# Optimization experiments

Hardware: AMD Instinct MI355X
Metric: run time of the kernel (lower is better)

Reference implementation:

```python
import jax, jax.numpy as jnp
import numpy as np

H, C, R, L = 4, 32, 4, 2   # heads, per-head dim, num_relations, num_layers
D = H * C                  # hidden_channels = in_channels = 128
EPS_BN = 1e-5
NEG_SLOPE = 0.2


def _forward(x0, src0, dst0, ea0, src1, dst1, ea1,
             Wl, Wr, bl, br, att, conv_b,
             bn_g, bn_b, bn_m, bn_v,
             skip_W, skip_b,
             proj_W, proj_b, pbn_g, pbn_b, pbn_m, pbn_v, prelu_a,
             n_t0, n_t1):
    x = x0
    layers = [(src0, dst0, ea0, n_t0), (src1, dst1, ea1, n_t1)]
    for i, (src, dst, ea, nt) in enumerate(layers):
        xt = x[:nt]                               # [nt, D] target nodes
        out = xt @ skip_W[i] + skip_b[i]          # skip connection
        for j in range(R):                        # per-relation GATv2 + BN (eval)
            mask = (ea == j)
            xl = (x @ Wl[i, j] + bl[i, j]).reshape(-1, H, C)   # [N, H, C]
            xr = (xt @ Wr[i, j] + br[i, j]).reshape(-1, H, C)  # [nt, H, C]
            msg = xl[src] + xr[dst]                            # [E, H, C]
            logit = jnp.sum(jax.nn.leaky_relu(msg, NEG_SLOPE) * att[i, j], axis=-1)  # [E, H]
            logit = jnp.where(mask[:, None], logit, -1e9)      # mask other relations
            amax = jax.ops.segment_max(logit, dst, num_segments=nt)                  # [nt, H]
            p = jnp.exp(logit - amax[dst]) * mask[:, None]
            denom = jax.ops.segment_sum(p, dst, num_segments=nt)
            alpha = p / jnp.maximum(denom, 1e-16)[dst]                               # [E, H]
            agg = jax.ops.segment_sum(alpha[..., None] * xl[src], dst, num_segments=nt)
            agg = agg.reshape(nt, D) + conv_b[i, j]
            out = out + (agg - bn_m[i, j]) * jax.lax.rsqrt(bn_v[i, j] + EPS_BN) * bn_g[i, j] + bn_b[i, j]
        x = jax.nn.elu(out)   # dropout is identity in eval mode
    # projection head: Linear -> BN(eval) -> PReLU -> Dropout(identity)
    h = x @ proj_W + proj_b
    h = (h - pbn_m) * jax.lax.rsqrt(pbn_v + EPS_BN) * pbn_g + pbn_b
    proj = jnp.where(h > 0, h, prelu_a * h)
    return x, proj


def setup_inputs() -> dict:
    key = jax.random.key(0)
    ks = jax.random.split(key, 32)
    N0, E0, N1, E1, N2 = 100000, 400000, 30000, 150000, 8000

    def w(k, shape, s=0.1):
        return jax.random.normal(k, shape, dtype=jnp.float32) * s

    return {
        'x0': jax.random.normal(ks[0], (N0, D), dtype=jnp.float32),
        'src0': jax.random.randint(ks[1], (E0,), 0, N0),
        'dst0': jax.random.randint(ks[2], (E0,), 0, N1),
        'ea0': jax.random.randint(ks[3], (E0,), 0, R),
        'src1': jax.random.randint(ks[4], (E1,), 0, N1),
        'dst1': jax.random.randint(ks[5], (E1,), 0, N2),
        'ea1': jax.random.randint(ks[6], (E1,), 0, R),
        'Wl': w(ks[7], (L, R, D, D)), 'Wr': w(ks[8], (L, R, D, D)),
        'bl': w(ks[9], (L, R, D)), 'br': w(ks[10], (L, R, D)),
        'att': w(ks[11], (L, R, H, C)), 'conv_b': w(ks[12], (L, R, D)),
        'bn_g': 1.0 + w(ks[13], (L, R, D)), 'bn_b': w(ks[14], (L, R, D)),
        'bn_m': w(ks[15], (L, R, D)),
        'bn_v': 0.5 + jax.random.uniform(ks[16], (L, R, D), dtype=jnp.float32),
        'skip_W': w(ks[17], (L, D, D)), 'skip_b': w(ks[18], (L, D)),
        'proj_W': w(ks[19], (D, D)), 'proj_b': w(ks[20], (D,)),
        'pbn_g': 1.0 + w(ks[21], (D,)), 'pbn_b': w(ks[22], (D,)),
        'pbn_m': w(ks[23], (D,)),
        'pbn_v': 0.5 + jax.random.uniform(ks[24], (D,), dtype=jnp.float32),
        'prelu_a': jnp.full((1,), 0.25, dtype=jnp.float32),
        'n_t0': N1, 'n_t1': N2,
    }


def reference(x0, src0, dst0, ea0, src1, dst1, ea1,
              Wl, Wr, bl, br, att, conv_b,
              bn_g, bn_b, bn_m, bn_v,
              skip_W, skip_b,
              proj_W, proj_b, pbn_g, pbn_b, pbn_m, pbn_v, prelu_a,
              n_t0, n_t1):
    return _forward(x0, src0, dst0, ea0, src1, dst1, ea1,
                    Wl, Wr, bl, br, att, conv_b,
                    bn_g, bn_b, bn_m, bn_v,
                    skip_W, skip_b,
                    proj_W, proj_b, pbn_g, pbn_b, pbn_m, pbn_v, prelu_a,
                    n_t0, n_t1)
```

## Files before the change

kernel.cpp:

```cpp
#include <hip/hip_runtime.h>
#include <stdint.h>

typedef short bf16x8 __attribute__((ext_vector_type(8)));
typedef float f32x4 __attribute__((ext_vector_type(4)));

constexpr float cEPS = 1e-5f;
constexpr float cSLOPE = 0.2f;

__device__ __forceinline__ unsigned short f2b(float f){
  unsigned u = __float_as_uint(f);
  u = (u + 0x7fffu + ((u >> 16) & 1u)) >> 16;
  return (unsigned short)u;
}
__device__ __forceinline__ float b2f(unsigned short b){
  return __uint_as_float(((unsigned)b) << 16);
}

__global__ void k_f32_to_bf16(const float* __restrict__ in, unsigned short* __restrict__ out, int n8){
  int i = blockIdx.x * 256 + threadIdx.x;
  if(i >= n8) return;
  float4 v0 = ((const float4*)in)[i*2];
  float4 v1 = ((const float4*)in)[i*2 + 1];
  bf16x8 o = { (short)f2b(v0.x), (short)f2b(v0.y), (short)f2b(v0.z), (short)f2b(v0.w),
               (short)f2b(v1.x), (short)f2b(v1.y), (short)f2b(v1.z), (short)f2b(v1.w) };
  ((bf16x8*)out)[i] = o;
}

__global__ void k_build_wt(const float* __restrict__ Wl, const float* __restrict__ Wr,
                           const float* __restrict__ skW, const float* __restrict__ pjW,
                           unsigned short* __restrict__ wt){
  int idx = blockIdx.x * 256 + threadIdx.x;
  if(idx >= 19 * 16384) return;
  int mat = idx >> 14, r = idx & 16383;
  int n = r >> 7, k = r & 127;
  const float* src;
  if(mat < 8)       src = Wl + mat * 16384;
  else if(mat < 16) src = Wr + (mat - 8) * 16384;
  else if(mat < 18) src = skW + (mat - 16) * 16384;
  else              src = pjW;
  wt[idx] = f2b(src[k * 128 + n]);
}

__global__ void k_hist_key(const int* __restrict__ dst, const int* __restrict__ ea,
                           unsigned int* __restrict__ cnt, int E){
  int i = blockIdx.x * 256 + threadIdx.x;
  if(i < E) atomicAdd(cnt + (dst[i]*4 + ea[i]), 1u);
}

__device__ __forceinline__ unsigned wave_iscan(unsigned v, int lane){
  #pragma unroll
  for(int ofs = 1; ofs < 64; ofs <<= 1){
    unsigned y = __shfl_up(v, ofs);
    if(lane >= ofs) v += y;
  }
  return v;
}

__global__ __launch_bounds__(256) void k_scan_partial(
    const unsigned int* __restrict__ cnt, unsigned int* __restrict__ off,
    unsigned int* __restrict__ bsum, int n){
  __shared__ unsigned int buf[4096];
  __shared__ unsigned int wofs[4];
  const int base = blockIdx.x * 4096;
  for(int i = threadIdx.x; i < 4096; i += 256){
    int idx = base + i;
    buf[i] = (idx < n) ? cnt[idx] : 0u;
  }
  __syncthreads();
  const int lane = threadIdx.x & 63, wid = threadIdx.x >> 6;
  const int b = threadIdx.x * 16;
  unsigned loc[16]; unsigned s = 0;
  #pragma unroll
  for(int i = 0; i < 16; ++i){ loc[i] = s; s += buf[b + i]; }
  unsigned isc = wave_iscan(s, lane);
  unsigned texc = isc - s;
  if(lane == 63) wofs[wid] = isc;
  __syncthreads();
  unsigned wbase = 0;
  for(int w = 0; w < wid; ++w) wbase += wofs[w];
  unsigned tbase = wbase + texc;
  #pragma unroll
  for(int i = 0; i < 16; ++i){
    int idx = base + b + i;
    if(idx < n) off[idx] = tbase + loc[i];
  }
  if(threadIdx.x == 255) bsum[blockIdx.x] = wbase + isc;
}

__global__ void k_scan_bsum(unsigned int* __restrict__ bsum, unsigned int* __restrict__ off,
                            int nblk, int n){
  if(threadIdx.x == 0 && blockIdx.x == 0){
    unsigned acc = 0;
    for(int i = 0; i < nblk; ++i){ unsigned v = bsum[i]; bsum[i] = acc; acc += v; }
    off[n] = acc;
  }
}

__global__ void k_scan_add(unsigned int* __restrict__ off, unsigned int* __restrict__ cur,
                           const unsigned int* __restrict__ bsum, int n){
  int i = blockIdx.x * 256 + threadIdx.x;
  if(i < n){
    unsigned v = off[i] + bsum[i >> 12];
    off[i] = v;
    cur[i] = v;
  }
}

__global__ void k_scatter_key(const int* __restrict__ dst, const int* __restrict__ ea,
                              const int* __restrict__ src,
                              unsigned int* __restrict__ cursor,
                              int* __restrict__ psrc, int E){
  int i = blockIdx.x * 256 + threadIdx.x;
  if(i < E){
    unsigned int pos = atomicAdd(cursor + (dst[i]*4 + ea[i]), 1u);
    psrc[pos] = src[i];
  }
}

template<bool OUT_BF16>
__global__ __launch_bounds__(256) void k_gemm(
    const unsigned short* __restrict__ A, int M,
    const unsigned short* __restrict__ wtBase, long wtStride,
    const float* __restrict__ biasBase, int biasStride,
    void* __restrict__ outBase, long outStride)
{
  __shared__ unsigned short lw[128 * 136];
  const unsigned short* Wt = wtBase + (long)blockIdx.y * wtStride;
  #pragma unroll
  for(int it = 0; it < 8; ++it){
    int idx = it * 256 + threadIdx.x;
    int row = idx >> 4, c8 = idx & 15;
    bf16x8 v = *(const bf16x8*)(Wt + row * 128 + c8 * 8);
    *(bf16x8*)(lw + row * 136 + c8 * 8) = v;
  }

  const float* bias = biasBase + (long)blockIdx.y * biasStride;
  const int wave = threadIdx.x >> 6, lane = threadIdx.x & 63;
  const int l16 = lane & 15, lhi = lane >> 4;

  const int row0 = blockIdx.x * 64 + wave * 16;
  const int arow = row0 + l16;
  const bf16x8 zf = {0,0,0,0,0,0,0,0};
  bf16x8 afr[4];
  if(arow < M){
    #pragma unroll
    for(int kb = 0; kb < 4; ++kb)
      afr[kb] = *(const bf16x8*)(A + (long)arow*128 + kb*32 + lhi*8);
  } else {
    #pragma unroll
    for(int kb = 0; kb < 4; ++kb) afr[kb] = zf;
  }
  __syncthreads();

  const f32x4 z4 = {0.f,0.f,0.f,0.f};
  f32x4 acc[8];
  #pragma unroll
  for(int cb = 0; cb < 8; ++cb) acc[cb] = z4;
  #pragma unroll
  for(int cb = 0; cb < 8; ++cb){
    #pragma unroll
    for(int kb = 0; kb < 4; ++kb){
      bf16x8 bfr = *(const bf16x8*)(lw + (cb*16 + l16)*136 + kb*32 + lhi*8);
      acc[cb] = __builtin_amdgcn_mfma_f32_16x16x32_bf16(afr[kb], bfr, acc[cb], 0, 0, 0);
    }
  }

  #pragma unroll
  for(int cb = 0; cb < 8; ++cb){
    int col = cb*16 + l16;
    float bv = bias[col];
    #pragma unroll
    for(int q = 0; q < 4; ++q){
      int rrow = row0 + lhi*4 + q;
      if(rrow < M){
        float v = acc[cb][q] + bv;
        long oidx = (long)blockIdx.y * outStride + (long)rrow * 128 + col;
        if(OUT_BF16) ((unsigned short*)outBase)[oidx] = f2b(v);
        else         ((float*)outBase)[oidx] = v;
      }
    }
  }
}

__global__ __launch_bounds__(256) void k_dst_agg(
    const unsigned int* __restrict__ off, const int* __restrict__ psrc,
    const unsigned short* __restrict__ xl, const unsigned short* __restrict__ xr,
    const float* __restrict__ att,
    const float* __restrict__ conv_b, const float* __restrict__ bn_g, const float* __restrict__ bn_b,
    const float* __restrict__ bn_m, const float* __restrict__ bn_v,
    float* __restrict__ out, int N, int nt)
{
  __shared__ float contrib[4][128];
  const int t = blockIdx.x;
  const int r = threadIdx.x >> 6;
  const int lane = threadIdx.x & 63;
  const int sub  = lane >> 4;
  const int l16  = lane & 15;

  const bf16x8 xrv = *(const bf16x8*)(xr + ((long)r*nt + t)*128 + l16*8);
  float xrf[8];
  #pragma unroll
  for(int q = 0; q < 8; ++q) xrf[q] = b2f((unsigned short)xrv[q]);
  const float4 a0 = ((const float4*)(att + r*128 + l16*8))[0];
  const float4 a1 = ((const float4*)(att + r*128 + l16*8))[1];
  const float av[8] = {a0.x,a0.y,a0.z,a0.w,a1.x,a1.y,a1.z,a1.w};

  const unsigned s0 = off[t*4 + r], s1 = off[t*4 + r + 1];

  float m = -3.0e38f, den = 0.f;
  float acc[8];
  #pragma unroll
  for(int q = 0; q < 8; ++q) acc[q] = 0.f;

  for(unsigned e = s0 + sub; e < s1; e += 4){
    int s = psrc[e];
    bf16x8 xlv = *(const bf16x8*)(xl + ((long)r*N + s)*128 + l16*8);
    float xlf[8];
    #pragma unroll
    for(int q = 0; q < 8; ++q) xlf[q] = b2f((unsigned short)xlv[q]);
    float part = 0.f;
    #pragma unroll
    for(int q = 0; q < 8; ++q){
      float v = xlf[q] + xrf[q];
      v = v >= 0.f ? v : cSLOPE * v;
      part += v * av[q];
    }
    part += __shfl_xor(part, 1);
    part += __shfl_xor(part, 2);
    float p;
    if(part > m + 8.f){
      float corr = __expf(m - part);
      den *= corr;
      #pragma unroll
      for(int q = 0; q < 8; ++q) acc[q] *= corr;
      m = part;
      p = 1.f;
    } else {
      p = __expf(part - m);
    }
    den += p;
    #pragma unroll
    for(int q = 0; q < 8; ++q) acc[q] += p * xlf[q];
  }

  #pragma unroll
  for(int ofs = 16; ofs <= 32; ofs <<= 1){
    float m2 = __shfl_xor(m, ofs);
    float d2 = __shfl_xor(den, ofs);
    float M = fmaxf(m, m2);
    float sA = __expf(m - M), sB = __expf(m2 - M);
    den = den * sA + d2 * sB;
    #pragma unroll
    for(int q = 0; q < 8; ++q){
      float a2 = __shfl_xor(acc[q], ofs);
      acc[q] = acc[q] * sA + a2 * sB;
    }
    m = M;
  }

  if(sub == 0){
    const float inv = 1.f / fmaxf(den, 1e-16f);
    #pragma unroll
    for(int q = 0; q < 8; ++q){
      int c = l16*8 + q;
      float cb = conv_b[r*128 + c], gg = bn_g[r*128 + c], bb = bn_b[r*128 + c];
      float mm = bn_m[r*128 + c],  vv = bn_v[r*128 + c];
      contrib[r][c] = (acc[q] * inv + cb - mm) * rsqrtf(vv + cEPS) * gg + bb;
    }
  }
  __syncthreads();
  if(threadIdx.x < 64){
    int c = threadIdx.x * 2;
    float2 o = *(float2*)(out + (long)t*128 + c);
    o.x += contrib[0][c]   + contrib[1][c]   + contrib[2][c]   + contrib[3][c];
    o.y += contrib[0][c+1] + contrib[1][c+1] + contrib[2][c+1] + contrib[3][c+1];
    *(float2*)(out + (long)t*128 + c) = o;
  }
}

__global__ void k_elu_act(const float* __restrict__ in, unsigned short* __restrict__ outBf,
                          float* __restrict__ outF32, int n4){
  int i = blockIdx.x * 256 + threadIdx.x;
  if(i >= n4) return;
  float4 v = ((const float4*)in)[i];
  float4 e;
  e.x = v.x > 0.f ? v.x : __expf(v.x) - 1.f;
  e.y = v.y > 0.f ? v.y : __expf(v.y) - 1.f;
  e.z = v.z > 0.f ? v.z : __expf(v.z) - 1.f;
  e.w = v.w > 0.f ? v.w : __expf(v.w) - 1.f;
  ushort4 o = { f2b(e.x), f2b(e.y), f2b(e.z), f2b(e.w) };
  ((ushort4*)outBf)[i] = o;
  if(outF32) ((float4*)outF32)[i] = e;
}

__global__ void k_pbn_prelu(float* __restrict__ hbuf, const float* __restrict__ g, const float* __restrict__ b,
                            const float* __restrict__ m, const float* __restrict__ v,
                            const float* __restrict__ a, int n4){
  int i = blockIdx.x * 256 + threadIdx.x;
  if(i >= n4) return;
  int c4 = i & 31;
  float4 x  = ((const float4*)hbuf)[i];
  float4 gg = ((const float4*)g)[c4], bb = ((const float4*)b)[c4];
  float4 mm = ((const float4*)m)[c4], vv = ((const float4*)v)[c4];
  float al = a[0];
  float4 y;
  y.x = (x.x - mm.x) * rsqrtf(vv.x + cEPS) * gg.x + bb.x; y.x = y.x > 0.f ? y.x : al * y.x;
  y.y = (x.y - mm.y) * rsqrtf(vv.y + cEPS) * gg.y + bb.y; y.y = y.y > 0.f ? y.y : al * y.y;
  y.z = (x.z - mm.z) * rsqrtf(vv.z + cEPS) * gg.z + bb.z; y.z = y.z > 0.f ? y.z : al * y.z;
  y.w = (x.w - mm.w) * rsqrtf(vv.w + cEPS) * gg.w + bb.w; y.w = y.w > 0.f ? y.w : al * y.w;
  ((float4*)hbuf)[i] = y;
}

extern "C" void kernel_launch(void* const* d_in, const int* in_sizes, int n_in,
                              void* d_out, int out_size, void* d_ws, size_t ws_size,
                              hipStream_t stream)
{
  const float* x0     = (const float*)d_in[0];
  const int*   src0   = (const int*)d_in[1];
  const int*   dst0   = (const int*)d_in[2];
  const int*   ea0    = (const int*)d_in[3];
  const int*   src1   = (const int*)d_in[4];
  const int*   dst1   = (const int*)d_in[5];
  const int*   ea1    = (const int*)d_in[6];
  const float* Wl     = (const float*)d_in[7];
  const float* Wr     = (const float*)d_in[8];
  const float* bl     = (const float*)d_in[9];
  const float* br     = (const float*)d_in[10];
  const float* att    = (const float*)d_in[11];
  const float* conv_b = (const float*)d_in[12];
  const float* bn_g   = (const float*)d_in[13];
  const float* bn_b   = (const float*)d_in[14];
  const float* bn_m   = (const float*)d_in[15];
  const float* bn_v   = (const float*)d_in[16];
  const float* skip_W = (const float*)d_in[17];
  const float* skip_b = (const float*)d_in[18];
  const float* proj_W = (const float*)d_in[19];
  const float* proj_b = (const float*)d_in[20];
  const float* pbn_g  = (const float*)d_in[21];
  const float* pbn_b  = (const float*)d_in[22];
  const float* pbn_m  = (const float*)d_in[23];
  const float* pbn_v  = (const float*)d_in[24];
  const float* prelu_a= (const float*)d_in[25];

  const int N0 = in_sizes[0] / 128;
  const int E0 = in_sizes[1];
  const int E1 = in_sizes[4];
  const int N1 = 30000;
  const int N2 = 8000;
  const int jc = 4;

  auto al = [](size_t x){ return (x + 255) & ~(size_t)255; };
  char* p = (char*)d_ws;
  auto carve = [&](size_t bytes){ char* r = p; p += al(bytes); return r; };
  unsigned short* wt    = (unsigned short*)carve((size_t)19*16384*2);
  unsigned short* xbf   = (unsigned short*)carve((size_t)N0*256);
  unsigned short* xlb   = (unsigned short*)carve((size_t)jc*N0*256);
  unsigned short* xrb   = (unsigned short*)carve((size_t)jc*N1*256);
  unsigned int*   cnt   = (unsigned int*)carve((size_t)(N1*4+1)*4);
  unsigned int*   off   = (unsigned int*)carve((size_t)(N1*4+1)*4);
  unsigned int*   cur   = (unsigned int*)carve((size_t)(N1*4+1)*4);
  unsigned int*   bsum  = (unsigned int*)carve((size_t)256*4);
  int*            psrc  = (int*)carve((size_t)E0*4);
  float*          out1  = (float*)carve((size_t)N1*512);

  k_f32_to_bf16<<<(N0*16 + 255)/256, 256, 0, stream>>>(x0, xbf, N0*16);
  k_build_wt<<<(19*16384 + 255)/256, 256, 0, stream>>>(Wl, Wr, skip_W, proj_W, wt);

  auto run_layer = [&](int li, int N, int nt, const int* src, const int* dst, const int* ea, int E){
    const int nbins = nt * 4;
    const int nblk = (nbins + 4095) / 4096;
    hipMemsetAsync(cnt, 0, (size_t)(nbins + 1) * 4, stream);
    k_hist_key<<<(E + 255)/256, 256, 0, stream>>>(dst, ea, cnt, E);
    k_scan_partial<<<nblk, 256, 0, stream>>>(cnt, off, bsum, nbins);
    k_scan_bsum<<<1, 64, 0, stream>>>(bsum, off, nblk, nbins);
    k_scan_add<<<(nbins + 255)/256, 256, 0, stream>>>(off, cur, bsum, nbins);
    k_scatter_key<<<(E + 255)/256, 256, 0, stream>>>(dst, ea, src, cur, psrc, E);

    k_gemm<false><<<dim3((nt+63)/64, 1), 256, 0, stream>>>(
        xbf, nt, wt + (16+li)*16384, 0, skip_b + li*128, 0, out1, 0);
    k_gemm<true><<<dim3((N+63)/64, jc), 256, 0, stream>>>(
        xbf, N,  wt + (li*4)*16384,   16384, bl + (li*4)*128, 128, xlb, (long)N*128);
    k_gemm<true><<<dim3((nt+63)/64, jc), 256, 0, stream>>>(
        xbf, nt, wt + (8+li*4)*16384, 16384, br + (li*4)*128, 128, xrb, (long)nt*128);
    k_dst_agg<<<nt, 256, 0, stream>>>(
        off, psrc, xlb, xrb, att + li*512,
        conv_b + li*512, bn_g + li*512, bn_b + li*512, bn_m + li*512, bn_v + li*512,
        out1, N, nt);
  };

  run_layer(0, N0, N1, src0, dst0, ea0, E0);
  k_elu_act<<<(N1*32 + 255)/256, 256, 0, stream>>>(out1, xbf, nullptr, N1*32);
  run_layer(1, N1, N2, src1, dst1, ea1, E1);

  float* outX = (float*)d_out;
  float* outP = (float*)d_out + (size_t)N2*128;
  k_elu_act<<<(N2*32 + 255)/256, 256, 0, stream>>>(out1, xbf, outX, N2*32);
  k_gemm<false><<<dim3((N2+63)/64, 1), 256, 0, stream>>>(
      xbf, N2, wt + 18*16384, 0, proj_b, 0, outP, 0);
  k_pbn_prelu<<<(N2*32 + 255)/256, 256, 0, stream>>>(outP, pbn_g, pbn_b, pbn_m, pbn_v, prelu_a, N2*32);
}
```

Measured before the change: 478.0 us.

## Fuse layer GEMMs, ELU, scan and projection epilogue to cut kernel launches

```diff
diff --git a/kernel.cpp b/kernel.cpp
--- a/kernel.cpp
+++ b/kernel.cpp
@@ -87,23 +87,18 @@
   if(threadIdx.x == 255) bsum[blockIdx.x] = wbase + isc;
 }
 
-__global__ void k_scan_bsum(unsigned int* __restrict__ bsum, unsigned int* __restrict__ off,
-                            int nblk, int n){
-  if(threadIdx.x == 0 && blockIdx.x == 0){
-    unsigned acc = 0;
-    for(int i = 0; i < nblk; ++i){ unsigned v = bsum[i]; bsum[i] = acc; acc += v; }
-    off[n] = acc;
-  }
-}
-
 __global__ void k_scan_add(unsigned int* __restrict__ off, unsigned int* __restrict__ cur,
-                           const unsigned int* __restrict__ bsum, int n){
+                           const unsigned int* __restrict__ bsum, const unsigned int* __restrict__ cnt,
+                           int n){
   int i = blockIdx.x * 256 + threadIdx.x;
-  if(i < n){
-    unsigned v = off[i] + bsum[i >> 12];
-    off[i] = v;
-    cur[i] = v;
-  }
+  if(i >= n) return;
+  int myblk = i >> 12;
+  unsigned base = 0;
+  for(int j = 0; j < myblk; ++j) base += bsum[j];
+  unsigned v = off[i] + base;
+  off[i] = v;
+  cur[i] = v;
+  if(i == n - 1) off[n] = v + cnt[i];
 }
 
 __global__ void k_scatter_key(const int* __restrict__ dst, const int* __restrict__ ea,
@@ -117,15 +112,30 @@
   }
 }
 
-template<bool OUT_BF16>
-__global__ __launch_bounds__(256) void k_gemm(
-    const unsigned short* __restrict__ A, int M,
-    const unsigned short* __restrict__ wtBase, long wtStride,
-    const float* __restrict__ biasBase, int biasStride,
-    void* __restrict__ outBase, long outStride)
+__global__ __launch_bounds__(256) void k_gemm_layer(
+    const unsigned short* __restrict__ A,
+    const unsigned short* __restrict__ wt,
+    const float* __restrict__ bl, const float* __restrict__ br, const float* __restrict__ skip_b,
+    unsigned short* __restrict__ xlb, unsigned short* __restrict__ xrb, float* __restrict__ out1,
+    int li, int N, int nt)
 {
+  const int y = blockIdx.y;
+  int M; const unsigned short* Wt; const float* bias;
+  unsigned short* outB = nullptr; float* outF = nullptr;
+  if(y < 4){
+    M = N;  Wt = wt + (li*4 + y)*16384;      bias = bl + (li*4 + y)*128;
+    outB = xlb + (long)y*N*128;
+  } else if(y < 8){
+    int r = y - 4;
+    M = nt; Wt = wt + (8 + li*4 + r)*16384;  bias = br + (li*4 + r)*128;
+    outB = xrb + (long)r*nt*128;
+  } else {
+    M = nt; Wt = wt + (16 + li)*16384;       bias = skip_b + li*128;
+    outF = out1;
+  }
+  if(blockIdx.x * 64 >= M) return;
+
   __shared__ unsigned short lw[128 * 136];
-  const unsigned short* Wt = wtBase + (long)blockIdx.y * wtStride;
   #pragma unroll
   for(int it = 0; it < 8; ++it){
     int idx = it * 256 + threadIdx.x;
@@ -134,10 +144,8 @@
     *(bf16x8*)(lw + row * 136 + c8 * 8) = v;
   }
 
-  const float* bias = biasBase + (long)blockIdx.y * biasStride;
   const int wave = threadIdx.x >> 6, lane = threadIdx.x & 63;
   const int l16 = lane & 15, lhi = lane >> 4;
-
   const int row0 = blockIdx.x * 64 + wave * 16;
   const int arow = row0 + l16;
   const bf16x8 zf = {0,0,0,0,0,0,0,0};
@@ -174,9 +182,71 @@
       int rrow = row0 + lhi*4 + q;
       if(rrow < M){
         float v = acc[cb][q] + bv;
-        long oidx = (long)blockIdx.y * outStride + (long)rrow * 128 + col;
-        if(OUT_BF16) ((unsigned short*)outBase)[oidx] = f2b(v);
-        else         ((float*)outBase)[oidx] = v;
+        long oidx = (long)rrow * 128 + col;
+        if(outB) outB[oidx] = f2b(v);
+        else     outF[oidx] = v;
+      }
+    }
+  }
+}
+
+__global__ __launch_bounds__(256) void k_gemm_proj(
+    const unsigned short* __restrict__ A, int M,
+    const unsigned short* __restrict__ Wt, const float* __restrict__ bias,
+    const float* __restrict__ pg, const float* __restrict__ pb,
+    const float* __restrict__ pm, const float* __restrict__ pv,
+    const float* __restrict__ pa, float* __restrict__ outP)
+{
+  __shared__ unsigned short lw[128 * 136];
+  #pragma unroll
+  for(int it = 0; it < 8; ++it){
+    int idx = it * 256 + threadIdx.x;
+    int row = idx >> 4, c8 = idx & 15;
+    bf16x8 v = *(const bf16x8*)(Wt + row * 128 + c8 * 8);
+    *(bf16x8*)(lw + row * 136 + c8 * 8) = v;
+  }
+  const int wave = threadIdx.x >> 6, lane = threadIdx.x & 63;
+  const int l16 = lane & 15, lhi = lane >> 4;
+  const int row0 = blockIdx.x * 64 + wave * 16;
+  const int arow = row0 + l16;
+  const bf16x8 zf = {0,0,0,0,0,0,0,0};
+  bf16x8 afr[4];
+  if(arow < M){
+    #pragma unroll
+    for(int kb = 0; kb < 4; ++kb)
+      afr[kb] = *(const bf16x8*)(A + (long)arow*128 + kb*32 + lhi*8);
+  } else {
+    #pragma unroll
+    for(int kb = 0; kb < 4; ++kb) afr[kb] = zf;
+  }
+  __syncthreads();
+
+  const f32x4 z4 = {0.f,0.f,0.f,0.f};
+  f32x4 acc[8];
+  #pragma unroll
+  for(int cb = 0; cb < 8; ++cb) acc[cb] = z4;
+  #pragma unroll
+  for(int cb = 0; cb < 8; ++cb){
+    #pragma unroll
+    for(int kb = 0; kb < 4; ++kb){
+      bf16x8 bfr = *(const bf16x8*)(lw + (cb*16 + l16)*136 + kb*32 + lhi*8);
+      acc[cb] = __builtin_amdgcn_mfma_f32_16x16x32_bf16(afr[kb], bfr, acc[cb], 0, 0, 0);
+    }
+  }
+  const float a0 = pa[0];
+  #pragma unroll
+  for(int cb = 0; cb < 8; ++cb){
+    int col = cb*16 + l16;
+    float bv = bias[col];
+    float gg = pg[col], bb = pb[col], mm = pm[col], vv = pv[col];
+    float rs = rsqrtf(vv + cEPS);
+    #pragma unroll
+    for(int q = 0; q < 4; ++q){
+      int rrow = row0 + lhi*4 + q;
+      if(rrow < M){
+        float h = (acc[cb][q] + bv - mm) * rs * gg + bb;
+        h = h > 0.f ? h : a0 * h;
+        outP[(long)rrow * 128 + col] = h;
       }
     }
   }
@@ -188,7 +258,8 @@
     const float* __restrict__ att,
     const float* __restrict__ conv_b, const float* __restrict__ bn_g, const float* __restrict__ bn_b,
     const float* __restrict__ bn_m, const float* __restrict__ bn_v,
-    float* __restrict__ out, int N, int nt)
+    const float* __restrict__ skipIn, unsigned short* __restrict__ outBf,
+    float* __restrict__ outF32, int N, int nt)
 {
   __shared__ float contrib[4][128];
   const int t = blockIdx.x;
@@ -271,44 +342,18 @@
   __syncthreads();
   if(threadIdx.x < 64){
     int c = threadIdx.x * 2;
-    float2 o = *(float2*)(out + (long)t*128 + c);
-    o.x += contrib[0][c]   + contrib[1][c]   + contrib[2][c]   + contrib[3][c];
-    o.y += contrib[0][c+1] + contrib[1][c+1] + contrib[2][c+1] + contrib[3][c+1];
-    *(float2*)(out + (long)t*128 + c) = o;
-  }
-}
-
-__global__ void k_elu_act(const float* __restrict__ in, unsigned short* __restrict__ outBf,
-                          float* __restrict__ outF32, int n4){
-  int i = blockIdx.x * 256 + threadIdx.x;
-  if(i >= n4) return;
-  float4 v = ((const float4*)in)[i];
-  float4 e;
-  e.x = v.x > 0.f ? v.x : __expf(v.x) - 1.f;
-  e.y = v.y > 0.f ? v.y : __expf(v.y) - 1.f;
-  e.z = v.z > 0.f ? v.z : __expf(v.z) - 1.f;
-  e.w = v.w > 0.f ? v.w : __expf(v.w) - 1.f;
-  ushort4 o = { f2b(e.x), f2b(e.y), f2b(e.z), f2b(e.w) };
-  ((ushort4*)outBf)[i] = o;
-  if(outF32) ((float4*)outF32)[i] = e;
-}
-
-__global__ void k_pbn_prelu(float* __restrict__ hbuf, const float* __restrict__ g, const float* __restrict__ b,
-                            const float* __restrict__ m, const float* __restrict__ v,
-                            const float* __restrict__ a, int n4){
-  int i = blockIdx.x * 256 + threadIdx.x;
-  if(i >= n4) return;
-  int c4 = i & 31;
-  float4 x  = ((const float4*)hbuf)[i];
-  float4 gg = ((const float4*)g)[c4], bb = ((const float4*)b)[c4];
-  float4 mm = ((const float4*)m)[c4], vv = ((const float4*)v)[c4];
-  float al = a[0];
-  float4 y;
-  y.x = (x.x - mm.x) * rsqrtf(vv.x + cEPS) * gg.x + bb.x; y.x = y.x > 0.f ? y.x : al * y.x;
-  y.y = (x.y - mm.y) * rsqrtf(vv.y + cEPS) * gg.y + bb.y; y.y = y.y > 0.f ? y.y : al * y.y;
-  y.z = (x.z - mm.z) * rsqrtf(vv.z + cEPS) * gg.z + bb.z; y.z = y.z > 0.f ? y.z : al * y.z;
-  y.w = (x.w - mm.w) * rsqrtf(vv.w + cEPS) * gg.w + bb.w; y.w = y.w > 0.f ? y.w : al * y.w;
-  ((float4*)hbuf)[i] = y;
+    float2 o = *(const float2*)(skipIn + (long)t*128 + c);
+    float ox = o.x + contrib[0][c]   + contrib[1][c]   + contrib[2][c]   + contrib[3][c];
+    float oy = o.y + contrib[0][c+1] + contrib[1][c+1] + contrib[2][c+1] + contrib[3][c+1];
+    ox = ox > 0.f ? ox : __expf(ox) - 1.f;
+    oy = oy > 0.f ? oy : __expf(oy) - 1.f;
+    ushort2 ob = { f2b(ox), f2b(oy) };
+    *(ushort2*)(outBf + (long)t*128 + c) = ob;
+    if(outF32){
+      float2 of = { ox, oy };
+      *(float2*)(outF32 + (long)t*128 + c) = of;
+    }
+  }
 }
 
 extern "C" void kernel_launch(void* const* d_in, const int* in_sizes, int n_in,
@@ -366,36 +411,30 @@
   k_f32_to_bf16<<<(N0*16 + 255)/256, 256, 0, stream>>>(x0, xbf, N0*16);
   k_build_wt<<<(19*16384 + 255)/256, 256, 0, stream>>>(Wl, Wr, skip_W, proj_W, wt);
 
-  auto run_layer = [&](int li, int N, int nt, const int* src, const int* dst, const int* ea, int E){
+  auto run_layer = [&](int li, int N, int nt, const int* src, const int* dst, const int* ea, int E,
+                       unsigned short* outBf, float* outF32){
     const int nbins = nt * 4;
     const int nblk = (nbins + 4095) / 4096;
     hipMemsetAsync(cnt, 0, (size_t)(nbins + 1) * 4, stream);
     k_hist_key<<<(E + 255)/256, 256, 0, stream>>>(dst, ea, cnt, E);
     k_scan_partial<<<nblk, 256, 0, stream>>>(cnt, off, bsum, nbins);
-    k_scan_bsum<<<1, 64, 0, stream>>>(bsum, off, nblk, nbins);
-    k_scan_add<<<(nbins + 255)/256, 256, 0, stream>>>(off, cur, bsum, nbins);
+    k_scan_add<<<(nbins + 255)/256, 256, 0, stream>>>(off, cur, bsum, cnt, nbins);
     k_scatter_key<<<(E + 255)/256, 256, 0, stream>>>(dst, ea, src, cur, psrc, E);
 
-    k_gemm<false><<<dim3((nt+63)/64, 1), 256, 0, stream>>>(
-        xbf, nt, wt + (16+li)*16384, 0, skip_b + li*128, 0, out1, 0);
-    k_gemm<true><<<dim3((N+63)/64, jc), 256, 0, stream>>>(
-        xbf, N,  wt + (li*4)*16384,   16384, bl + (li*4)*128, 128, xlb, (long)N*128);
-    k_gemm<true><<<dim3((nt+63)/64, jc), 256, 0, stream>>>(
-        xbf, nt, wt + (8+li*4)*16384, 16384, br + (li*4)*128, 128, xrb, (long)nt*128);
+    k_gemm_layer<<<dim3((N + 63)/64, 9), 256, 0, stream>>>(
+        xbf, wt, bl, br, skip_b, xlb, xrb, out1, li, N, nt);
     k_dst_agg<<<nt, 256, 0, stream>>>(
         off, psrc, xlb, xrb, att + li*512,
         conv_b + li*512, bn_g + li*512, bn_b + li*512, bn_m + li*512, bn_v + li*512,
-        out1, N, nt);
+        out1, outBf, outF32, N, nt);
   };
-
-  run_layer(0, N0, N1, src0, dst0, ea0, E0);
-  k_elu_act<<<(N1*32 + 255)/256, 256, 0, stream>>>(out1, xbf, nullptr, N1*32);
-  run_layer(1, N1, N2, src1, dst1, ea1, E1);
 
   float* outX = (float*)d_out;
   float* outP = (float*)d_out + (size_t)N2*128;
-  k_elu_act<<<(N2*32 + 255)/256, 256, 0, stream>>>(out1, xbf, outX, N2*32);
-  k_gemm<false><<<dim3((N2+63)/64, 1), 256, 0, stream>>>(
-      xbf, N2, wt + 18*16384, 0, proj_b, 0, outP, 0);
-  k_pbn_prelu<<<(N2*32 + 255)/256, 256, 0, stream>>>(outP, pbn_g, pbn_b, pbn_m, pbn_v, prelu_a, N2*32);
-}
+
+  run_layer(0, N0, N1, src0, dst0, ea0, E0, xbf, nullptr);
+  run_layer(1, N1, N2, src1, dst1, ea1, E1, xbf, outX);
+
+  k_gemm_proj<<<(N2 + 63)/64, 256, 0, stream>>>(
+      xbf, N2, wt + 18*16384, proj_b, pbn_g, pbn_b, pbn_m, pbn_v, prelu_a, outP);
+}
```

Measured after the change: 448.2 us. 6.2% less time.
